# Kernel tuning notes

Hardware: AMD Instinct MI355X
Metric: run time of the kernel (lower is better)

The kernel has to match this reference:

```python
import jax, jax.numpy as jnp
import numpy as np

E, T, I, O = 8, 8192, 2048, 4096  # experts, total_tokens, in_features, out_features


def setup_inputs() -> dict:
    key = jax.random.key(0)
    k1, k2, k3 = jax.random.split(key, 3)
    inputs = jax.random.normal(k1, (T, I), dtype=jnp.float32)
    # lecun_normal-style scale for the (E, I, O) kernel (fan_in = I)
    kernel = jax.random.normal(k2, (E, I, O), dtype=jnp.float32) * (1.0 / np.float32(np.sqrt(I)))
    # nonzero bias so the ragged bias-expansion path is exercised
    bias = jax.random.normal(k3, (E, O), dtype=jnp.float32) * 0.02
    # tokens are sorted by expert; equal groups summing exactly to T
    group_sizes = jnp.full((E,), T // E, dtype=jnp.int32)
    return {"inputs": inputs, "group_sizes": group_sizes, "kernel": kernel, "bias": bias}


def reference(inputs, group_sizes, kernel, bias):
    # Ragged grouped GEMM: row block g of `inputs` (size group_sizes[g]) is
    # multiplied by kernel[g] of shape (I, O). Matches _ragged_dot with
    # out_first=False: contraction dims ((1,), (1,)), rhs group dim 0.
    out = jax.lax.ragged_dot(inputs, kernel, group_sizes)  # (T, O)
    # Per-group bias add: bias[e] broadcast over that expert's token block.
    expert_ids = jnp.repeat(jnp.arange(E), group_sizes, total_repeat_length=T)
    return out + bias[expert_ids]
```

## Files before the change

kernel.cpp:

```cpp
#include <hip/hip_runtime.h>


typedef short bf16x8 __attribute__((ext_vector_type(8)));
typedef float f32x4 __attribute__((ext_vector_type(4)));
typedef unsigned short u16x4 __attribute__((ext_vector_type(4)));
typedef unsigned short u16x8 __attribute__((ext_vector_type(8)));

constexpr int Ecnt = 8;
constexpr int Ttok = 8192;
constexpr int Ifeat = 2048;
constexpr int Ofeat = 4096;

constexpr int BM = 256, BN = 256, BK = 64;
constexpr int NKT = Ifeat / BK;
constexpr int RTE = (Ttok / Ecnt) / BM;
constexpr int CTN = Ofeat / BN;
constexpr int NTILE = Ecnt * RTE * CTN;
constexpr int QCAP = NTILE / 8;

__device__ __forceinline__ unsigned short f2bf(float f) {
  unsigned u = __float_as_uint(f);
  unsigned r = (u + 0x7FFFu + ((u >> 16) & 1u)) >> 16;
  return (unsigned short)r;
}

__global__ __launch_bounds__(256) void cvt_a(const float* __restrict__ src,
                                             unsigned short* __restrict__ dst,
                                             int* __restrict__ qcnt) {
  size_t i = ((size_t)blockIdx.x * 256 + threadIdx.x) * 4;
  float4 f = *(const float4*)(src + i);
  u16x4 v;
  v[0] = f2bf(f.x); v[1] = f2bf(f.y); v[2] = f2bf(f.z); v[3] = f2bf(f.w);
  *(u16x4*)(dst + i) = v;
  if (blockIdx.x == 0 && threadIdx.x < 8) qcnt[threadIdx.x] = 0;
}

__global__ __launch_bounds__(256) void cvt_b(const float* __restrict__ src,
                                             unsigned short* __restrict__ dst) {
  constexpr int LDST = 129;
  __shared__ float tile[64 * LDST];
  const int e = blockIdx.z;
  const int i0 = blockIdx.y * 64;
  const int o0 = blockIdx.x * 128;
  const int tid = threadIdx.x;
  {
    const int tx = tid & 31, ty = tid >> 5;
    const float* s = src + ((size_t)e * Ifeat + i0) * Ofeat + o0 + tx * 4;
#pragma unroll
    for (int r = 0; r < 8; ++r) {
      int i = r * 8 + ty;
      float4 f = *(const float4*)(s + (size_t)i * Ofeat);
      float* l = tile + i * LDST + tx * 4;
      l[0] = f.x; l[1] = f.y; l[2] = f.z; l[3] = f.w;
    }
  }
  __syncthreads();
  {
    const int ic = (tid & 7) * 8;
    const int oc = tid >> 3;
#pragma unroll
    for (int p = 0; p < 4; ++p) {
      int o = p * 32 + oc;
      u16x8 v;
#pragma unroll
      for (int j = 0; j < 8; ++j) v[j] = f2bf(tile[(ic + j) * LDST + o]);
      unsigned short* d =
          dst + ((size_t)e * Ofeat + o0 + o) * Ifeat + i0 + ic;
      *(u16x8*)d = v;
    }
  }
}

__device__ __forceinline__ void ld16(const unsigned short* g, unsigned short* l) {
  __builtin_amdgcn_global_load_lds(
      (const __attribute__((address_space(1))) unsigned int*)g,
      (__attribute__((address_space(3))) unsigned int*)l, 16, 0, 0);
}

__global__ __launch_bounds__(512, 2) void moe_gemm(
    const unsigned short* __restrict__ A,
    const unsigned short* __restrict__ Bt,
    const int* __restrict__ gs,
    const float* __restrict__ bias,
    float* __restrict__ C,
    int* __restrict__ qcnt) {
  __shared__ unsigned short lA[2][BM * BK];
  __shared__ unsigned short lB[2][BN * BK];
  __shared__ int s_tile;

  const int tid = threadIdx.x;

  if (tid == 0) {
    unsigned xcc = __builtin_amdgcn_s_getreg(63508) & 7;
    int t = 0;
#pragma unroll
    for (int a = 0; a < 8; ++a) {
      int qq = (xcc + a) & 7;
      int ix = atomicAdd(&qcnt[qq], 1);
      if (ix < QCAP) { t = (qq << 6) | ix; break; }
    }
    s_tile = t;
  }
  __syncthreads();

  const int tcode = s_tile;
  const int q = tcode >> 6;
  const int idx = tcode & 63;
  const int rt = idx & (RTE - 1);
  const int ct = idx >> 2;
  const int row0 = q * (Ttok / Ecnt) + rt * BM;
  const int col0 = ct * BN;

  int e = 0;
  {
    int cum = 0;
#pragma unroll
    for (int g = 0; g < Ecnt; ++g) {
      int s = gs[g];
      if (row0 >= cum + s) { cum += s; e = g + 1; }
    }
  }

  const unsigned short* __restrict__ Ag = A + (size_t)row0 * Ifeat;
  const unsigned short* __restrict__ Bg = Bt + ((size_t)e * Ofeat + col0) * Ifeat;

  int64_t goff[4];
  int lof[4];
#pragma unroll
  for (int p = 0; p < 4; ++p) {
    const int c = tid + p * 512;
    const int r = c >> 3, kcp = c & 7;
    goff[p] = (int64_t)r * Ifeat + ((kcp ^ (r & 7)) << 3);
    lof[p] = c << 3;
  }

  const int wave = tid >> 6, lane = tid & 63;
  const int wr = wave >> 2, wc = wave & 3;
  const int lrow = lane & 15;
  const int kg = lane >> 4;
  const int xr = lrow & 7;
  const int aslot0 = (kg ^ xr) << 3;
  const int aslot1 = ((4 + kg) ^ xr) << 3;
  const int arbase = (wr * 128 + lrow) * BK;
  const int brbase = (wc * 64 + lrow) * BK;

  f32x4 acc[8][4];
#pragma unroll
  for (int i = 0; i < 8; ++i)
#pragma unroll
    for (int jj = 0; jj < 4; ++jj) acc[i][jj] = (f32x4){0.f, 0.f, 0.f, 0.f};

#pragma unroll
  for (int p = 0; p < 4; ++p) ld16(Ag + goff[p], &lA[0][lof[p]]);
#pragma unroll
  for (int p = 0; p < 4; ++p) ld16(Bg + goff[p], &lB[0][lof[p]]);
  __syncthreads();

#define AFRAG(MT, SL) (*(const bf16x8*)(al + arbase + (MT) * (16 * BK) + (SL)))
#define MFMA_QUAD(MT0, MT1)                                                  \
  __builtin_amdgcn_s_barrier();                                              \
  __builtin_amdgcn_s_setprio(1);                                             \
  _Pragma("unroll") for (int nt = 0; nt < 4; ++nt) {                         \
    acc[MT0][nt] = __builtin_amdgcn_mfma_f32_16x16x32_bf16(                  \
        a00, bf[nt][0], acc[MT0][nt], 0, 0, 0);                              \
    acc[MT0][nt] = __builtin_amdgcn_mfma_f32_16x16x32_bf16(                  \
        a01, bf[nt][1], acc[MT0][nt], 0, 0, 0);                              \
    acc[MT1][nt] = __builtin_amdgcn_mfma_f32_16x16x32_bf16(                  \
        a10, bf[nt][0], acc[MT1][nt], 0, 0, 0);                              \
    acc[MT1][nt] = __builtin_amdgcn_mfma_f32_16x16x32_bf16(                  \
        a11, bf[nt][1], acc[MT1][nt], 0, 0, 0);                              \
  }                                                                          \
  __builtin_amdgcn_s_setprio(0);

  int cur = 0;
  for (int kt = 0; kt < NKT; ++kt) {
    const unsigned short* al = lA[cur];
    const unsigned short* bl = lB[cur];
    unsigned short* an = lA[cur ^ 1];
    unsigned short* bn = lB[cur ^ 1];
    const int64_t kn = (int64_t)(kt + 1) * BK;
    const bool pf = (kt + 1 < NKT);

    bf16x8 bf[4][2];
#pragma unroll
    for (int nt = 0; nt < 4; ++nt) {
      bf[nt][0] = *(const bf16x8*)(bl + brbase + nt * (16 * BK) + aslot0);
      bf[nt][1] = *(const bf16x8*)(bl + brbase + nt * (16 * BK) + aslot1);
    }

    {
      bf16x8 a00 = AFRAG(0, aslot0), a01 = AFRAG(0, aslot1);
      bf16x8 a10 = AFRAG(1, aslot0), a11 = AFRAG(1, aslot1);
      if (pf) {
        ld16(Ag + goff[0] + kn, an + lof[0]);
        ld16(Ag + goff[1] + kn, an + lof[1]);
        ld16(Ag + goff[2] + kn, an + lof[2]);
        ld16(Ag + goff[3] + kn, an + lof[3]);
      }
      MFMA_QUAD(0, 1)
      __builtin_amdgcn_s_barrier();
    }
    {
      bf16x8 a00 = AFRAG(2, aslot0), a01 = AFRAG(2, aslot1);
      bf16x8 a10 = AFRAG(3, aslot0), a11 = AFRAG(3, aslot1);
      if (pf) {
        ld16(Bg + goff[0] + kn, bn + lof[0]);
        ld16(Bg + goff[1] + kn, bn + lof[1]);
        ld16(Bg + goff[2] + kn, bn + lof[2]);
        ld16(Bg + goff[3] + kn, bn + lof[3]);
      }
      MFMA_QUAD(2, 3)
      __builtin_amdgcn_s_barrier();
    }
    {
      bf16x8 a00 = AFRAG(4, aslot0), a01 = AFRAG(4, aslot1);
      bf16x8 a10 = AFRAG(5, aslot0), a11 = AFRAG(5, aslot1);
      MFMA_QUAD(4, 5)
      __builtin_amdgcn_s_barrier();
    }
    {
      bf16x8 a00 = AFRAG(6, aslot0), a01 = AFRAG(6, aslot1);
      bf16x8 a10 = AFRAG(7, aslot0), a11 = AFRAG(7, aslot1);
      MFMA_QUAD(6, 7)
    }
    __syncthreads();
    cur ^= 1;
  }
#undef AFRAG
#undef MFMA_QUAD

  const int r0 = (lane >> 4) * 4;
  const int cc = lane & 15;
  const float* be = bias + (size_t)e * Ofeat;
#pragma unroll
  for (int mt = 0; mt < 8; ++mt) {
    const int row = row0 + wr * 128 + mt * 16 + r0;
#pragma unroll
    for (int nt = 0; nt < 4; ++nt) {
      const int col = col0 + wc * 64 + nt * 16 + cc;
      const float b = be[col];
      float* Cp = C + (size_t)row * Ofeat + col;
#pragma unroll
      for (int r = 0; r < 4; ++r) Cp[(size_t)r * Ofeat] = acc[mt][nt][r] + b;
    }
  }
}

extern "C" void kernel_launch(void* const* d_in, const int* in_sizes, int n_in,
                              void* d_out, int out_size, void* d_ws, size_t ws_size,
                              hipStream_t stream) {
  const float* inputs = (const float*)d_in[0];
  const int* group_sizes = (const int*)d_in[1];
  const float* kern = (const float*)d_in[2];
  const float* bias = (const float*)d_in[3];
  float* out = (float*)d_out;

  unsigned short* Abf = (unsigned short*)d_ws;
  unsigned short* Bbf = Abf + (size_t)Ttok * Ifeat;
  const size_t cnt_off = (size_t)Ttok * Ifeat * 2 + (size_t)Ecnt * Ofeat * Ifeat * 2;
  int* qcnt = (int*)((char*)d_ws + cnt_off);

  cvt_a<<<(Ttok * (size_t)Ifeat) / (4 * 256), 256, 0, stream>>>(inputs, Abf, qcnt);
  cvt_b<<<dim3(Ofeat / 128, Ifeat / 64, Ecnt), 256, 0, stream>>>(kern, Bbf);

  moe_gemm<<<NTILE, 512, 0, stream>>>(Abf, Bbf, group_sizes, bias, out, qcnt);
}
```

Baseline: 623.2 us.

## Switch GEMM mainloop to 4-stage BK=32 pipeline with explicit vmcnt waits

The K tile shrinks from 64 to 32 and the LDS double buffer becomes a 4-deep ring. Global-to-LDS loads run three stages ahead, with explicit s_waitcnt vmcnt counts and sched_barriers in place of a full __syncthreads per iteration. The LDS layout and swizzle are reworked so each 32-wide K slice packs two rows per 64-element line, and fragment offsets are precomputed. The aim is to hide global latency better while keeping LDS usage the same, at the cost of twice as many loop iterations and barriers, plus hand-tuned wait counts that could be fragile.

```diff
diff --git a/kernel.cpp b/kernel.cpp
--- a/kernel.cpp
+++ b/kernel.cpp
@@ -11,8 +11,9 @@
 constexpr int Ifeat = 2048;
 constexpr int Ofeat = 4096;
 
-constexpr int BM = 256, BN = 256, BK = 64;
+constexpr int BM = 256, BN = 256, BK = 32;
 constexpr int NKT = Ifeat / BK;
+constexpr int NBUF = 4;
 constexpr int RTE = (Ttok / Ecnt) / BM;
 constexpr int CTN = Ofeat / BN;
 constexpr int NTILE = Ecnt * RTE * CTN;
@@ -84,8 +85,8 @@
     const float* __restrict__ bias,
     float* __restrict__ C,
     int* __restrict__ qcnt) {
-  __shared__ unsigned short lA[2][BM * BK];
-  __shared__ unsigned short lB[2][BN * BK];
+  __shared__ unsigned short lA[NBUF][BM * BK];
+  __shared__ unsigned short lB[NBUF][BN * BK];
   __shared__ int s_tile;
 
   const int tid = threadIdx.x;
@@ -124,25 +125,32 @@
   const unsigned short* __restrict__ Ag = A + (size_t)row0 * Ifeat;
   const unsigned short* __restrict__ Bg = Bt + ((size_t)e * Ofeat + col0) * Ifeat;
 
-  int64_t goff[4];
-  int lof[4];
-#pragma unroll
-  for (int p = 0; p < 4; ++p) {
-    const int c = tid + p * 512;
-    const int r = c >> 3, kcp = c & 7;
-    goff[p] = (int64_t)r * Ifeat + ((kcp ^ (r & 7)) << 3);
-    lof[p] = c << 3;
+  int64_t soff[2];
+  int lof[2];
+#pragma unroll
+  for (int p = 0; p < 2; ++p) {
+    const int f = tid + p * 512;
+    const int l = f >> 3;
+    const int ls = (f & 7) ^ (l & 7);
+    const int r = 2 * l + (ls >> 2);
+    const int kc = ls & 3;
+    soff[p] = (int64_t)r * Ifeat + kc * 8;
+    lof[p] = f * 8;
   }
 
   const int wave = tid >> 6, lane = tid & 63;
   const int wr = wave >> 2, wc = wave & 3;
   const int lrow = lane & 15;
   const int kg = lane >> 4;
-  const int xr = lrow & 7;
-  const int aslot0 = (kg ^ xr) << 3;
-  const int aslot1 = ((4 + kg) ^ xr) << 3;
-  const int arbase = (wr * 128 + lrow) * BK;
-  const int brbase = (wc * 64 + lrow) * BK;
+
+  auto frd = [&](int R) {
+    return (R >> 1) * 64 + (((((R & 1) << 2) | kg) ^ ((R >> 1) & 7)) << 3);
+  };
+  int aoff[8], boff[4];
+#pragma unroll
+  for (int mt = 0; mt < 8; ++mt) aoff[mt] = frd(wr * 128 + mt * 16 + lrow);
+#pragma unroll
+  for (int nt = 0; nt < 4; ++nt) boff[nt] = frd(wc * 64 + nt * 16 + lrow);
 
   f32x4 acc[8][4];
 #pragma unroll
@@ -150,84 +158,81 @@
 #pragma unroll
     for (int jj = 0; jj < 4; ++jj) acc[i][jj] = (f32x4){0.f, 0.f, 0.f, 0.f};
 
-#pragma unroll
-  for (int p = 0; p < 4; ++p) ld16(Ag + goff[p], &lA[0][lof[p]]);
-#pragma unroll
-  for (int p = 0; p < 4; ++p) ld16(Bg + goff[p], &lB[0][lof[p]]);
-  __syncthreads();
-
-#define AFRAG(MT, SL) (*(const bf16x8*)(al + arbase + (MT) * (16 * BK) + (SL)))
-#define MFMA_QUAD(MT0, MT1)                                                  \
-  __builtin_amdgcn_s_barrier();                                              \
-  __builtin_amdgcn_s_setprio(1);                                             \
-  _Pragma("unroll") for (int nt = 0; nt < 4; ++nt) {                         \
-    acc[MT0][nt] = __builtin_amdgcn_mfma_f32_16x16x32_bf16(                  \
-        a00, bf[nt][0], acc[MT0][nt], 0, 0, 0);                              \
-    acc[MT0][nt] = __builtin_amdgcn_mfma_f32_16x16x32_bf16(                  \
-        a01, bf[nt][1], acc[MT0][nt], 0, 0, 0);                              \
-    acc[MT1][nt] = __builtin_amdgcn_mfma_f32_16x16x32_bf16(                  \
-        a10, bf[nt][0], acc[MT1][nt], 0, 0, 0);                              \
-    acc[MT1][nt] = __builtin_amdgcn_mfma_f32_16x16x32_bf16(                  \
-        a11, bf[nt][1], acc[MT1][nt], 0, 0, 0);                              \
-  }                                                                          \
-  __builtin_amdgcn_s_setprio(0);
-
-  int cur = 0;
-  for (int kt = 0; kt < NKT; ++kt) {
-    const unsigned short* al = lA[cur];
-    const unsigned short* bl = lB[cur];
-    unsigned short* an = lA[cur ^ 1];
-    unsigned short* bn = lB[cur ^ 1];
-    const int64_t kn = (int64_t)(kt + 1) * BK;
-    const bool pf = (kt + 1 < NKT);
-
-    bf16x8 bf[4][2];
-#pragma unroll
-    for (int nt = 0; nt < 4; ++nt) {
-      bf[nt][0] = *(const bf16x8*)(bl + brbase + nt * (16 * BK) + aslot0);
-      bf[nt][1] = *(const bf16x8*)(bl + brbase + nt * (16 * BK) + aslot1);
-    }
+#define STAGE_A(BUF, KT)                                      \
+  ld16(Ag + soff[0] + (int64_t)(KT) * BK, &lA[BUF][lof[0]]);  \
+  ld16(Ag + soff[1] + (int64_t)(KT) * BK, &lA[BUF][lof[1]]);
+#define STAGE_B(BUF, KT)                                      \
+  ld16(Bg + soff[0] + (int64_t)(KT) * BK, &lB[BUF][lof[0]]);  \
+  ld16(Bg + soff[1] + (int64_t)(KT) * BK, &lB[BUF][lof[1]]);
+
+  STAGE_A(0, 0) STAGE_B(0, 0)
+  STAGE_A(1, 1) STAGE_B(1, 1)
+  STAGE_A(2, 2) STAGE_B(2, 2)
+  asm volatile("s_waitcnt vmcnt(8)" ::: "memory");
+  __builtin_amdgcn_s_barrier();
+  __builtin_amdgcn_sched_barrier(0);
+
+  for (int t = 0; t < NKT; ++t) {
+    const unsigned short* la = &lA[t & 3][0];
+    const unsigned short* lb = &lB[t & 3][0];
+    const bool pf = (t + 3 < NKT);
+    const int nb = (t + 3) & 3;
+
+    bf16x8 bq[4];
+#pragma unroll
+    for (int nt = 0; nt < 4; ++nt) bq[nt] = *(const bf16x8*)(lb + boff[nt]);
 
     {
-      bf16x8 a00 = AFRAG(0, aslot0), a01 = AFRAG(0, aslot1);
-      bf16x8 a10 = AFRAG(1, aslot0), a11 = AFRAG(1, aslot1);
-      if (pf) {
-        ld16(Ag + goff[0] + kn, an + lof[0]);
-        ld16(Ag + goff[1] + kn, an + lof[1]);
-        ld16(Ag + goff[2] + kn, an + lof[2]);
-        ld16(Ag + goff[3] + kn, an + lof[3]);
+      bf16x8 aq[4];
+#pragma unroll
+      for (int mt = 0; mt < 4; ++mt) aq[mt] = *(const bf16x8*)(la + aoff[mt]);
+      if (pf) { STAGE_A(nb, t + 3) }
+      __builtin_amdgcn_s_barrier();
+      asm volatile("s_waitcnt lgkmcnt(0)" ::: "memory");
+      __builtin_amdgcn_sched_barrier(0);
+      __builtin_amdgcn_s_setprio(1);
+#pragma unroll
+      for (int mt = 0; mt < 4; ++mt)
+#pragma unroll
+        for (int nt = 0; nt < 4; ++nt)
+          acc[mt][nt] = __builtin_amdgcn_mfma_f32_16x16x32_bf16(
+              aq[mt], bq[nt], acc[mt][nt], 0, 0, 0);
+      __builtin_amdgcn_s_setprio(0);
+      __builtin_amdgcn_s_barrier();
+    }
+    {
+      bf16x8 aq[4];
+#pragma unroll
+      for (int mt = 0; mt < 4; ++mt)
+        aq[mt] = *(const bf16x8*)(la + aoff[4 + mt]);
+      if (pf) { STAGE_B(nb, t + 3) }
+      __builtin_amdgcn_s_barrier();
+      asm volatile("s_waitcnt lgkmcnt(0)" ::: "memory");
+      __builtin_amdgcn_sched_barrier(0);
+      __builtin_amdgcn_s_setprio(1);
+#pragma unroll
+      for (int mt = 0; mt < 4; ++mt)
+#pragma unroll
+        for (int nt = 0; nt < 4; ++nt)
+          acc[4 + mt][nt] = __builtin_amdgcn_mfma_f32_16x16x32_bf16(
+              aq[mt], bq[nt], acc[4 + mt][nt], 0, 0, 0);
+      __builtin_amdgcn_s_setprio(0);
+    }
+
+    if (t < NKT - 1) {
+      if (t < NKT - 3) {
+        asm volatile("s_waitcnt vmcnt(8)" ::: "memory");
+      } else if (t == NKT - 3) {
+        asm volatile("s_waitcnt vmcnt(4)" ::: "memory");
+      } else {
+        asm volatile("s_waitcnt vmcnt(0)" ::: "memory");
       }
-      MFMA_QUAD(0, 1)
-      __builtin_amdgcn_s_barrier();
-    }
-    {
-      bf16x8 a00 = AFRAG(2, aslot0), a01 = AFRAG(2, aslot1);
-      bf16x8 a10 = AFRAG(3, aslot0), a11 = AFRAG(3, aslot1);
-      if (pf) {
-        ld16(Bg + goff[0] + kn, bn + lof[0]);
-        ld16(Bg + goff[1] + kn, bn + lof[1]);
-        ld16(Bg + goff[2] + kn, bn + lof[2]);
-        ld16(Bg + goff[3] + kn, bn + lof[3]);
-      }
-      MFMA_QUAD(2, 3)
-      __builtin_amdgcn_s_barrier();
-    }
-    {
-      bf16x8 a00 = AFRAG(4, aslot0), a01 = AFRAG(4, aslot1);
-      bf16x8 a10 = AFRAG(5, aslot0), a11 = AFRAG(5, aslot1);
-      MFMA_QUAD(4, 5)
-      __builtin_amdgcn_s_barrier();
-    }
-    {
-      bf16x8 a00 = AFRAG(6, aslot0), a01 = AFRAG(6, aslot1);
-      bf16x8 a10 = AFRAG(7, aslot0), a11 = AFRAG(7, aslot1);
-      MFMA_QUAD(6, 7)
-    }
-    __syncthreads();
-    cur ^= 1;
-  }
-#undef AFRAG
-#undef MFMA_QUAD
+      __builtin_amdgcn_s_barrier();
+      __builtin_amdgcn_sched_barrier(0);
+    }
+  }
+#undef STAGE_A
+#undef STAGE_B
 
   const int r0 = (lane >> 4) * 4;
   const int cc = lane & 15;
```

New measurement: 615.2 us. Within noise of the previous version (-1.3%).
